# Kernel optimization log

Hardware: AMD Instinct MI355X
Metric: run time of the kernel (lower is better)

Reference implementation:

```python
import jax, jax.numpy as jnp
import numpy as np

TEMPERATURE = 0.07
EPS = 1e-12  # matches torch F.normalize default eps


def setup_inputs() -> dict:
    key = jax.random.key(0)
    k1, k2 = jax.random.split(key)
    features1 = jax.random.normal(k1, (16384, 512), dtype=jnp.float32)
    features2 = jax.random.normal(k2, (16384, 512), dtype=jnp.float32)
    return {"features1": features1, "features2": features2}


def _l2_normalize(x):
    # torch F.normalize: x / max(||x||, eps)
    norm = jnp.sqrt(jnp.sum(x * x, axis=1, keepdims=True))
    return x / jnp.maximum(norm, EPS)


def reference(features1, features2):
    f1 = _l2_normalize(features1)
    f2 = _l2_normalize(features2)
    # [N, N] similarity logits
    logits = jnp.einsum('nd,md->nm', f1, f2) / TEMPERATURE
    n = logits.shape[0]
    # cross-entropy with labels = arange(n): mean over rows of (logsumexp - diag logit)
    log_probs = jax.nn.log_softmax(logits, axis=1)
    diag = jnp.diagonal(log_probs)
    loss = -jnp.mean(diag)
    return loss
```

## Files before the change

### kernel.cpp

```cpp
#include <hip/hip_runtime.h>
#include <stdint.h>

#define NROWS 16384
#define KDIM  512
#define BM 256
#define BN 128
#define CT 4
#define NCHUNK 32
#define NPH 16
#define INV_T 14.285714285714286f
#define LOG2E 1.4426950408889634f
#define LN2   0.6931471805599453f

typedef __bf16 bf16x8 __attribute__((ext_vector_type(8)));
typedef float  f32x16 __attribute__((ext_vector_type(16)));
typedef unsigned short u16x8 __attribute__((ext_vector_type(8)));

__device__ __forceinline__ void gload_lds16(const void* gptr, void* lptr) {
    uint32_t loff = (uint32_t)(uintptr_t)lptr;
    loff = __builtin_amdgcn_readfirstlane(loff);
    __builtin_amdgcn_global_load_lds(
        (const uint32_t __attribute__((address_space(1)))*)(uintptr_t)gptr,
        (uint32_t __attribute__((address_space(3)))*)(uintptr_t)loff,
        16, 0, 0);
}


__global__ void k_norm(const float* __restrict__ X, char* __restrict__ Y, float scale) {
    const int row  = blockIdx.x * 4 + (threadIdx.x >> 6);
    const int lane = threadIdx.x & 63;
    const float* xr = X + (size_t)row * KDIM + lane * 8;
    float4 a = *(const float4*)xr;
    float4 b = *(const float4*)(xr + 4);
    float ss = a.x*a.x + a.y*a.y + a.z*a.z + a.w*a.w
             + b.x*b.x + b.y*b.y + b.z*b.z + b.w*b.w;
    #pragma unroll
    for (int off = 1; off < 64; off <<= 1) ss += __shfl_xor(ss, off);
    const float s = scale / fmaxf(sqrtf(ss), 1e-12f);
    __bf16 o[8];
    o[0] = (__bf16)(a.x * s); o[1] = (__bf16)(a.y * s);
    o[2] = (__bf16)(a.z * s); o[3] = (__bf16)(a.w * s);
    o[4] = (__bf16)(b.x * s); o[5] = (__bf16)(b.y * s);
    o[6] = (__bf16)(b.z * s); o[7] = (__bf16)(b.w * s);
    const int kh = lane >> 2, q = lane & 3;
    const size_t gr = ((size_t)(kh * 512 + (row >> 5)) * 2 + (q >> 1)) * 64
                    + ((q & 1) << 5) + (row & 31);
    *(u16x8*)(Y + gr * 16) = *(const u16x8*)o;
}

__global__ __launch_bounds__(512, 1) void k_gemm(const char* __restrict__ A,
                                                 const char* __restrict__ B,
                                                 float* __restrict__ S_part) {
    __shared__ __align__(16) char L[4 * 24576];
    __shared__ float rowsum[2][BM];
    char* Lc = (char*)L;

    const int tid  = threadIdx.x;
    const int lane = tid & 63;
    const int w    = tid >> 6;
    const int wr   = w >> 1, wc = w & 1;
    const int bid  = blockIdx.x;
    const int xcd  = bid & 7;
    const int idx  = bid >> 3;
    const int st   = idx >> 5;
    const int wsub = idx & 31;
    const int sg   = xcd * 8 + st;
    const int bg   = sg & 7, cg = sg >> 3;
    const int brow  = (bg * 8 + (wsub >> 2)) * BM;
    const int chunk = cg * 4 + (wsub & 3);
    const int rbA0 = brow >> 5;

#define STGA(KH_, S_) do {                                                    \
        const char* g_ = A + ((size_t)((KH_) * 512 + rbA0) * 2048) + tid * 16;\
        char* l_ = Lc + (S_) * 24576 + tid * 16;                              \
        gload_lds16(g_,        l_);                                           \
        gload_lds16(g_ + 8192, l_ + 8192);                                    \
    } while (0)

#define STGB(KH_, S_) do {                                                    \
        const char* g_ = B + ((size_t)((KH_) * 512 + rbB0) * 2048) + tid * 16;\
        char* l_ = Lc + (S_) * 24576 + 16384 + tid * 16;                      \
        gload_lds16(g_, l_);                                                  \
    } while (0)

#define RDS(SET_, HH_) do {                                                   \
        const char* sl_ = Lc + ((HH_) & 3) * 24576;                           \
        _Pragma("unroll") for (int m_ = 0; m_ < 2; ++m_)                      \
        _Pragma("unroll") for (int ks_ = 0; ks_ < 2; ++ks_)                   \
            af[SET_][m_][ks_] = *(const bf16x8*)(sl_ + ((wr * 2 + m_) << 11)  \
                                           + (ks_ << 10) + (lane << 4));      \
        _Pragma("unroll") for (int n_ = 0; n_ < 2; ++n_)                      \
        _Pragma("unroll") for (int ks_ = 0; ks_ < 2; ++ks_)                   \
            bf[SET_][n_][ks_] = *(const bf16x8*)(sl_ + 16384                  \
                  + ((wc * 2 + n_) << 11) + (ks_ << 10) + (lane << 4));       \
    } while (0)

#define MM(SET_) do {                                                         \
        __builtin_amdgcn_s_setprio(1);                                        \
        _Pragma("unroll") for (int m_ = 0; m_ < 2; ++m_)                      \
        _Pragma("unroll") for (int n_ = 0; n_ < 2; ++n_)                      \
        _Pragma("unroll") for (int ks_ = 0; ks_ < 2; ++ks_)                   \
            acc[m_][n_] = __builtin_amdgcn_mfma_f32_32x32x16_bf16(            \
                af[SET_][m_][ks_], bf[SET_][n_][ks_], acc[m_][n_], 0, 0, 0);  \
        __builtin_amdgcn_s_setprio(0);                                        \
    } while (0)

    float rowacc = 0.f;
    #pragma unroll 1
    for (int ct = 0; ct < CT; ++ct) {
        const int rbB0 = (chunk * 16 + ct * 4);
        f32x16 acc[2][2] = {};
        bf16x8 af[2][2][2], bf[2][2][2];

        STGA(0, 0); STGB(0, 0);
        STGA(1, 1); STGB(1, 1);
        STGA(2, 2); STGB(2, 2);
        asm volatile("s_waitcnt vmcnt(3)" ::: "memory");
        __builtin_amdgcn_s_barrier();
        RDS(0, 0);

        #pragma unroll
        for (int h = 0; h < NPH; ++h) {
            if (h < NPH - 1) RDS((h + 1) & 1, h + 1);
            if (h < NPH - 3) { STGA(h + 3, (h + 3) & 3); STGB(h + 3, (h + 3) & 3); }
            MM(h & 1);
            if (h < NPH - 3)       asm volatile("s_waitcnt vmcnt(3)" ::: "memory");
            else if (h == NPH - 3) asm volatile("s_waitcnt vmcnt(0)" ::: "memory");
            __builtin_amdgcn_s_barrier();
        }

        #pragma unroll
        for (int m = 0; m < 2; ++m) {
            float rs[16];
            #pragma unroll
            for (int r = 0; r < 16; ++r)
                rs[r] = __builtin_amdgcn_exp2f(acc[m][0][r])
                      + __builtin_amdgcn_exp2f(acc[m][1][r]);
            #pragma unroll
            for (int off = 16; off >= 1; off >>= 1)
                #pragma unroll
                for (int r = 0; r < 16; ++r)
                    rs[r] += __shfl_xor(rs[r], off);
            if ((lane & 31) == 0) {
                const int rb = wr * 64 + m * 32 + (lane >> 5) * 4;
                #pragma unroll
                for (int r = 0; r < 16; ++r)
                    rowsum[wc][rb + (r & 3) + 8 * (r >> 2)] = rs[r];
            }
        }
        __syncthreads();
        if (tid < BM) rowacc += rowsum[0][tid] + rowsum[1][tid];
        __syncthreads();
    }
#undef STGA
#undef STGB
#undef RDS
#undef MM
    if (tid < BM) S_part[(size_t)chunk * NROWS + brow + tid] = rowacc;
}

__global__ void k_diag(const char* __restrict__ A, const char* __restrict__ B,
                       float* __restrict__ diag) {
    const int row  = blockIdx.x * 4 + (threadIdx.x >> 6);
    const int lane = threadIdx.x & 63;
    const int kh = lane >> 2, q = lane & 3;
    const size_t gr = ((size_t)(kh * 512 + (row >> 5)) * 2 + (q >> 1)) * 64
                    + ((q & 1) << 5) + (row & 31);
    const bf16x8 va = *(const bf16x8*)(A + gr * 16);
    const bf16x8 vb = *(const bf16x8*)(B + gr * 16);
    float d = 0.f;
    #pragma unroll
    for (int i = 0; i < 8; ++i) d += (float)va[i] * (float)vb[i];
    #pragma unroll
    for (int off2 = 1; off2 < 64; off2 <<= 1) d += __shfl_xor(d, off2);
    if (lane == 0) diag[row] = d;
}

__global__ void k_loss(const float* __restrict__ S_part, const float* __restrict__ diag,
                       float* __restrict__ partial) {
    const int g = blockIdx.x * 256 + threadIdx.x;
    float S = 0.f;
    #pragma unroll
    for (int c = 0; c < NCHUNK; ++c) S += S_part[(size_t)c * NROWS + g];
    float v = logf(S) - diag[g] * LN2;
    __shared__ float wsum[4];
    #pragma unroll
    for (int off = 1; off < 64; off <<= 1) v += __shfl_xor(v, off);
    if ((threadIdx.x & 63) == 0) wsum[threadIdx.x >> 6] = v;
    __syncthreads();
    if (threadIdx.x == 0) partial[blockIdx.x] = wsum[0] + wsum[1] + wsum[2] + wsum[3];
}

__global__ void k_final(const float* __restrict__ partial, float* __restrict__ out) {
    float v = partial[threadIdx.x];
    #pragma unroll
    for (int off = 1; off < 64; off <<= 1) v += __shfl_xor(v, off);
    if (threadIdx.x == 0) out[0] = v * (1.0f / (float)NROWS);
}

extern "C" void kernel_launch(void* const* d_in, const int* in_sizes, int n_in,
                              void* d_out, int out_size, void* d_ws, size_t ws_size,
                              hipStream_t stream) {
    const float* f1 = (const float*)d_in[0];
    const float* f2 = (const float*)d_in[1];
    float* out = (float*)d_out;

    char* ws = (char*)d_ws;
    char*  f1p   = ws;
    char*  f2p   = ws + (16u << 20);
    float* S_part = (float*)(ws + (32u << 20));
    float* diag   = (float*)(ws + (34u << 20));
    float* part   = (float*)(ws + (34u << 20) + (1u << 16));

    k_norm<<<dim3(NROWS / 4), dim3(256), 0, stream>>>(f1, f1p, INV_T * LOG2E);
    k_norm<<<dim3(NROWS / 4), dim3(256), 0, stream>>>(f2, f2p, 1.0f);
    k_gemm<<<dim3((NROWS / BM) * NCHUNK), dim3(512), 0, stream>>>(f1p, f2p, S_part);
    k_diag<<<dim3(NROWS / 4), dim3(256), 0, stream>>>(f1p, f2p, diag);
    k_loss<<<dim3(NROWS / 256), dim3(256), 0, stream>>>(S_part, diag, part);
    k_final<<<dim3(1), dim3(64), 0, stream>>>(part, out);
}
```

Before: 358.4 us.

## Reshape GEMM tile to 128x256 with 256-thread blocks, two per CU

```diff
diff --git a/kernel.cpp b/kernel.cpp
--- a/kernel.cpp
+++ b/kernel.cpp
@@ -3,11 +3,12 @@
 
 #define NROWS 16384
 #define KDIM  512
-#define BM 256
-#define BN 128
-#define CT 4
+#define BM 128
+#define BN 256
+#define CT 2
 #define NCHUNK 32
 #define NPH 16
+#define SLOT 24576
 #define INV_T 14.285714285714286f
 #define LOG2E 1.4426950408889634f
 #define LN2   0.6931471805599453f
@@ -48,10 +49,10 @@
     *(u16x8*)(Y + gr * 16) = *(const u16x8*)o;
 }
 
-__global__ __launch_bounds__(512, 1) void k_gemm(const char* __restrict__ A,
+__global__ __launch_bounds__(256, 2) void k_gemm(const char* __restrict__ A,
                                                  const char* __restrict__ B,
                                                  float* __restrict__ S_part) {
-    __shared__ __align__(16) char L[4 * 24576];
+    __shared__ __align__(16) char L[3 * SLOT];
     __shared__ float rowsum[2][BM];
     char* Lc = (char*)L;
 
@@ -64,68 +65,69 @@
     const int idx  = bid >> 3;
     const int st   = idx >> 5;
     const int wsub = idx & 31;
-    const int sg   = xcd * 8 + st;
-    const int bg   = sg & 7, cg = sg >> 3;
+    const int sg   = xcd * 16 + st;
+    const int bg   = sg & 15, cg = sg >> 4;
     const int brow  = (bg * 8 + (wsub >> 2)) * BM;
     const int chunk = cg * 4 + (wsub & 3);
     const int rbA0 = brow >> 5;
 
 #define STGA(KH_, S_) do {                                                    \
         const char* g_ = A + ((size_t)((KH_) * 512 + rbA0) * 2048) + tid * 16;\
-        char* l_ = Lc + (S_) * 24576 + tid * 16;                              \
+        char* l_ = Lc + (S_) * SLOT + tid * 16;                               \
         gload_lds16(g_,        l_);                                           \
-        gload_lds16(g_ + 8192, l_ + 8192);                                    \
+        gload_lds16(g_ + 4096, l_ + 4096);                                    \
     } while (0)
 
 #define STGB(KH_, S_) do {                                                    \
         const char* g_ = B + ((size_t)((KH_) * 512 + rbB0) * 2048) + tid * 16;\
-        char* l_ = Lc + (S_) * 24576 + 16384 + tid * 16;                      \
-        gload_lds16(g_, l_);                                                  \
-    } while (0)
-
-#define RDS(SET_, HH_) do {                                                   \
-        const char* sl_ = Lc + ((HH_) & 3) * 24576;                           \
+        char* l_ = Lc + (S_) * SLOT + 8192 + tid * 16;                        \
+        gload_lds16(g_,         l_);                                          \
+        gload_lds16(g_ +  4096, l_ +  4096);                                  \
+        gload_lds16(g_ +  8192, l_ +  8192);                                  \
+        gload_lds16(g_ + 12288, l_ + 12288);                                  \
+    } while (0)
+
+#define RDS(HH_) do {                                                         \
+        const char* sl_ = Lc + ((HH_) % 3) * SLOT;                            \
         _Pragma("unroll") for (int m_ = 0; m_ < 2; ++m_)                      \
         _Pragma("unroll") for (int ks_ = 0; ks_ < 2; ++ks_)                   \
-            af[SET_][m_][ks_] = *(const bf16x8*)(sl_ + ((wr * 2 + m_) << 11)  \
+            af[m_][ks_] = *(const bf16x8*)(sl_ + ((wr * 2 + m_) << 11)        \
                                            + (ks_ << 10) + (lane << 4));      \
-        _Pragma("unroll") for (int n_ = 0; n_ < 2; ++n_)                      \
+        _Pragma("unroll") for (int n_ = 0; n_ < 4; ++n_)                      \
         _Pragma("unroll") for (int ks_ = 0; ks_ < 2; ++ks_)                   \
-            bf[SET_][n_][ks_] = *(const bf16x8*)(sl_ + 16384                  \
-                  + ((wc * 2 + n_) << 11) + (ks_ << 10) + (lane << 4));       \
-    } while (0)
-
-#define MM(SET_) do {                                                         \
+            bf[n_][ks_] = *(const bf16x8*)(sl_ + 8192                         \
+                  + ((wc * 4 + n_) << 11) + (ks_ << 10) + (lane << 4));       \
+    } while (0)
+
+#define MM() do {                                                             \
         __builtin_amdgcn_s_setprio(1);                                        \
         _Pragma("unroll") for (int m_ = 0; m_ < 2; ++m_)                      \
-        _Pragma("unroll") for (int n_ = 0; n_ < 2; ++n_)                      \
+        _Pragma("unroll") for (int n_ = 0; n_ < 4; ++n_)                      \
         _Pragma("unroll") for (int ks_ = 0; ks_ < 2; ++ks_)                   \
             acc[m_][n_] = __builtin_amdgcn_mfma_f32_32x32x16_bf16(            \
-                af[SET_][m_][ks_], bf[SET_][n_][ks_], acc[m_][n_], 0, 0, 0);  \
+                af[m_][ks_], bf[n_][ks_], acc[m_][n_], 0, 0, 0);              \
         __builtin_amdgcn_s_setprio(0);                                        \
     } while (0)
 
     float rowacc = 0.f;
     #pragma unroll 1
     for (int ct = 0; ct < CT; ++ct) {
-        const int rbB0 = (chunk * 16 + ct * 4);
-        f32x16 acc[2][2] = {};
-        bf16x8 af[2][2][2], bf[2][2][2];
+        const int rbB0 = chunk * 16 + ct * 8;
+        f32x16 acc[2][4] = {};
+        bf16x8 af[2][2], bf[4][2];
 
         STGA(0, 0); STGB(0, 0);
         STGA(1, 1); STGB(1, 1);
-        STGA(2, 2); STGB(2, 2);
-        asm volatile("s_waitcnt vmcnt(3)" ::: "memory");
+        asm volatile("s_waitcnt vmcnt(6)" ::: "memory");
         __builtin_amdgcn_s_barrier();
-        RDS(0, 0);
 
         #pragma unroll
         for (int h = 0; h < NPH; ++h) {
-            if (h < NPH - 1) RDS((h + 1) & 1, h + 1);
-            if (h < NPH - 3) { STGA(h + 3, (h + 3) & 3); STGB(h + 3, (h + 3) & 3); }
-            MM(h & 1);
-            if (h < NPH - 3)       asm volatile("s_waitcnt vmcnt(3)" ::: "memory");
-            else if (h == NPH - 3) asm volatile("s_waitcnt vmcnt(0)" ::: "memory");
+            RDS(h);
+            if (h < NPH - 2) { STGA(h + 2, (h + 2) % 3); STGB(h + 2, (h + 2) % 3); }
+            MM();
+            if (h < NPH - 2)       asm volatile("s_waitcnt vmcnt(6)" ::: "memory");
+            else if (h == NPH - 2) asm volatile("s_waitcnt vmcnt(0)" ::: "memory");
             __builtin_amdgcn_s_barrier();
         }
 
@@ -135,7 +137,9 @@
             #pragma unroll
             for (int r = 0; r < 16; ++r)
                 rs[r] = __builtin_amdgcn_exp2f(acc[m][0][r])
-                      + __builtin_amdgcn_exp2f(acc[m][1][r]);
+                      + __builtin_amdgcn_exp2f(acc[m][1][r])
+                      + __builtin_amdgcn_exp2f(acc[m][2][r])
+                      + __builtin_amdgcn_exp2f(acc[m][3][r]);
             #pragma unroll
             for (int off = 16; off >= 1; off >>= 1)
                 #pragma unroll
@@ -214,7 +218,7 @@
 
     k_norm<<<dim3(NROWS / 4), dim3(256), 0, stream>>>(f1, f1p, INV_T * LOG2E);
     k_norm<<<dim3(NROWS / 4), dim3(256), 0, stream>>>(f2, f2p, 1.0f);
-    k_gemm<<<dim3((NROWS / BM) * NCHUNK), dim3(512), 0, stream>>>(f1p, f2p, S_part);
+    k_gemm<<<dim3((NROWS / BM) * NCHUNK), dim3(256), 0, stream>>>(f1p, f2p, S_part);
     k_diag<<<dim3(NROWS / 4), dim3(256), 0, stream>>>(f1p, f2p, diag);
     k_loss<<<dim3(NROWS / 256), dim3(256), 0, stream>>>(S_part, diag, part);
     k_final<<<dim3(1), dim3(64), 0, stream>>>(part, out);
```

New measurement: 350.2 us. -2.3%, faster.

## Switch similarity GEMM to FP8 MFMA with fp32 diagonal computed from raw inputs

Applied to the files above, without the earlier changes.

```diff
diff --git a/kernel.cpp b/kernel.cpp
--- a/kernel.cpp
+++ b/kernel.cpp
@@ -7,14 +7,14 @@
 #define BN 128
 #define CT 4
 #define NCHUNK 32
-#define NPH 16
+#define NPH 8
+#define SLOT 24576
 #define INV_T 14.285714285714286f
 #define LOG2E 1.4426950408889634f
-#define LN2   0.6931471805599453f
-
-typedef __bf16 bf16x8 __attribute__((ext_vector_type(8)));
-typedef float  f32x16 __attribute__((ext_vector_type(16)));
-typedef unsigned short u16x8 __attribute__((ext_vector_type(8)));
+
+typedef int   i32x4 __attribute__((ext_vector_type(4)));
+typedef int   i32x8 __attribute__((ext_vector_type(8)));
+typedef float f32x16 __attribute__((ext_vector_type(16)));
 
 __device__ __forceinline__ void gload_lds16(const void* gptr, void* lptr) {
     uint32_t loff = (uint32_t)(uintptr_t)lptr;
@@ -23,6 +23,34 @@
         (const uint32_t __attribute__((address_space(1)))*)(uintptr_t)gptr,
         (uint32_t __attribute__((address_space(3)))*)(uintptr_t)loff,
         16, 0, 0);
+}
+
+__device__ __forceinline__ uint32_t f2fp8_manual(float x) {
+    uint32_t b = __float_as_uint(x);
+    uint32_t s = (b >> 31) << 7;
+    uint32_t mag = b & 0x7FFFFFFFu;
+    if (mag >= 0x43E00000u) return s | 0x7Eu;
+    if (mag < 0x3C000000u) {
+        float m = __uint_as_float(mag) * 512.0f;
+        return s | (uint32_t)(m + 0.5f);
+    }
+    uint32_t r = mag + 0x0007FFFFu + ((mag >> 20) & 1u);
+    int e = (int)(r >> 23) - 120;
+    uint32_t m3 = (r >> 20) & 7u;
+    if (e <= 0) { float m = __uint_as_float(mag) * 512.0f; return s | (uint32_t)(m + 0.5f); }
+    if (e > 15 || (e == 15 && m3 == 7)) return s | 0x7Eu;
+    return s | ((uint32_t)e << 3) | m3;
+}
+
+__device__ __forceinline__ uint32_t pack4_fp8(float a, float b, float c, float d) {
+#if __has_builtin(__builtin_amdgcn_cvt_pk_fp8_f32)
+    int w = __builtin_amdgcn_cvt_pk_fp8_f32(a, b, 0, false);
+    w = __builtin_amdgcn_cvt_pk_fp8_f32(c, d, w, true);
+    return (uint32_t)w;
+#else
+    return f2fp8_manual(a) | (f2fp8_manual(b) << 8)
+         | (f2fp8_manual(c) << 16) | (f2fp8_manual(d) << 24);
+#endif
 }
 
 
@@ -37,21 +65,22 @@
     #pragma unroll
     for (int off = 1; off < 64; off <<= 1) ss += __shfl_xor(ss, off);
     const float s = scale / fmaxf(sqrtf(ss), 1e-12f);
-    __bf16 o[8];
-    o[0] = (__bf16)(a.x * s); o[1] = (__bf16)(a.y * s);
-    o[2] = (__bf16)(a.z * s); o[3] = (__bf16)(a.w * s);
-    o[4] = (__bf16)(b.x * s); o[5] = (__bf16)(b.y * s);
-    o[6] = (__bf16)(b.z * s); o[7] = (__bf16)(b.w * s);
-    const int kh = lane >> 2, q = lane & 3;
-    const size_t gr = ((size_t)(kh * 512 + (row >> 5)) * 2 + (q >> 1)) * 64
-                    + ((q & 1) << 5) + (row & 31);
-    *(u16x8*)(Y + gr * 16) = *(const u16x8*)o;
+    uint32_t w0 = pack4_fp8(a.x * s, a.y * s, a.z * s, a.w * s);
+    uint32_t w1 = pack4_fp8(b.x * s, b.y * s, b.z * s, b.w * s);
+    const int kt   = lane >> 3;
+    const int mlan = ((lane >> 2) & 1) * 32 + (row & 31);
+    const int half = (lane >> 1) & 1;
+    const int boff = (lane & 1) * 8;
+    char* dst = Y + ((size_t)(kt * 512 + (row >> 5)) * 2048)
+                  + half * 1024 + mlan * 16 + boff;
+    *(uint32_t*)dst = w0;
+    *(uint32_t*)(dst + 4) = w1;
 }
 
 __global__ __launch_bounds__(512, 1) void k_gemm(const char* __restrict__ A,
                                                  const char* __restrict__ B,
                                                  float* __restrict__ S_part) {
-    __shared__ __align__(16) char L[4 * 24576];
+    __shared__ __align__(16) char L[3 * SLOT];
     __shared__ float rowsum[2][BM];
     char* Lc = (char*)L;
 
@@ -70,62 +99,64 @@
     const int chunk = cg * 4 + (wsub & 3);
     const int rbA0 = brow >> 5;
 
-#define STGA(KH_, S_) do {                                                    \
-        const char* g_ = A + ((size_t)((KH_) * 512 + rbA0) * 2048) + tid * 16;\
-        char* l_ = Lc + (S_) * 24576 + tid * 16;                              \
+#define STGA(KT_, S_) do {                                                    \
+        const char* g_ = A + ((size_t)((KT_) * 512 + rbA0) * 2048) + tid * 16;\
+        char* l_ = Lc + (S_) * SLOT + tid * 16;                               \
         gload_lds16(g_,        l_);                                           \
         gload_lds16(g_ + 8192, l_ + 8192);                                    \
     } while (0)
 
-#define STGB(KH_, S_) do {                                                    \
-        const char* g_ = B + ((size_t)((KH_) * 512 + rbB0) * 2048) + tid * 16;\
-        char* l_ = Lc + (S_) * 24576 + 16384 + tid * 16;                      \
+#define STGB(KT_, S_) do {                                                    \
+        const char* g_ = B + ((size_t)((KT_) * 512 + rbB0) * 2048) + tid * 16;\
+        char* l_ = Lc + (S_) * SLOT + 16384 + tid * 16;                       \
         gload_lds16(g_, l_);                                                  \
     } while (0)
 
-#define RDS(SET_, HH_) do {                                                   \
-        const char* sl_ = Lc + ((HH_) & 3) * 24576;                           \
-        _Pragma("unroll") for (int m_ = 0; m_ < 2; ++m_)                      \
-        _Pragma("unroll") for (int ks_ = 0; ks_ < 2; ++ks_)                   \
-            af[SET_][m_][ks_] = *(const bf16x8*)(sl_ + ((wr * 2 + m_) << 11)  \
-                                           + (ks_ << 10) + (lane << 4));      \
-        _Pragma("unroll") for (int n_ = 0; n_ < 2; ++n_)                      \
-        _Pragma("unroll") for (int ks_ = 0; ks_ < 2; ++ks_)                   \
-            bf[SET_][n_][ks_] = *(const bf16x8*)(sl_ + 16384                  \
-                  + ((wc * 2 + n_) << 11) + (ks_ << 10) + (lane << 4));       \
-    } while (0)
-
-#define MM(SET_) do {                                                         \
+#define RDS(HH_) do {                                                         \
+        const char* sl_ = Lc + ((HH_) % 3) * SLOT;                            \
+        _Pragma("unroll") for (int m_ = 0; m_ < 2; ++m_) {                    \
+            i32x4 lo_ = *(const i32x4*)(sl_ + ((wr * 2 + m_) << 11) + (lane << 4));       \
+            i32x4 hi_ = *(const i32x4*)(sl_ + ((wr * 2 + m_) << 11) + 1024 + (lane << 4));\
+            _Pragma("unroll") for (int j_ = 0; j_ < 4; ++j_) {                \
+                aI[m_][j_] = lo_[j_]; aI[m_][4 + j_] = hi_[j_]; }             \
+        }                                                                     \
+        _Pragma("unroll") for (int n_ = 0; n_ < 2; ++n_) {                    \
+            i32x4 lo_ = *(const i32x4*)(sl_ + 16384 + ((wc * 2 + n_) << 11) + (lane << 4));       \
+            i32x4 hi_ = *(const i32x4*)(sl_ + 16384 + ((wc * 2 + n_) << 11) + 1024 + (lane << 4));\
+            _Pragma("unroll") for (int j_ = 0; j_ < 4; ++j_) {                \
+                bI[n_][j_] = lo_[j_]; bI[n_][4 + j_] = hi_[j_]; }             \
+        }                                                                     \
+    } while (0)
+
+#define MM() do {                                                             \
         __builtin_amdgcn_s_setprio(1);                                        \
         _Pragma("unroll") for (int m_ = 0; m_ < 2; ++m_)                      \
         _Pragma("unroll") for (int n_ = 0; n_ < 2; ++n_)                      \
-        _Pragma("unroll") for (int ks_ = 0; ks_ < 2; ++ks_)                   \
-            acc[m_][n_] = __builtin_amdgcn_mfma_f32_32x32x16_bf16(            \
-                af[SET_][m_][ks_], bf[SET_][n_][ks_], acc[m_][n_], 0, 0, 0);  \
+            acc[m_][n_] = __builtin_amdgcn_mfma_scale_f32_32x32x64_f8f6f4(    \
+                aI[m_], bI[n_], acc[m_][n_], 0, 0,                            \
+                0, 0x7F7F7F7F, 0, 0x7F7F7F7F);                                \
         __builtin_amdgcn_s_setprio(0);                                        \
     } while (0)
 
     float rowacc = 0.f;
     #pragma unroll 1
     for (int ct = 0; ct < CT; ++ct) {
-        const int rbB0 = (chunk * 16 + ct * 4);
+        const int rbB0 = chunk * 16 + ct * 4;
         f32x16 acc[2][2] = {};
-        bf16x8 af[2][2][2], bf[2][2][2];
+        i32x8 aI[2], bI[2];
 
         STGA(0, 0); STGB(0, 0);
         STGA(1, 1); STGB(1, 1);
-        STGA(2, 2); STGB(2, 2);
         asm volatile("s_waitcnt vmcnt(3)" ::: "memory");
         __builtin_amdgcn_s_barrier();
-        RDS(0, 0);
 
         #pragma unroll
         for (int h = 0; h < NPH; ++h) {
-            if (h < NPH - 1) RDS((h + 1) & 1, h + 1);
-            if (h < NPH - 3) { STGA(h + 3, (h + 3) & 3); STGB(h + 3, (h + 3) & 3); }
-            MM(h & 1);
-            if (h < NPH - 3)       asm volatile("s_waitcnt vmcnt(3)" ::: "memory");
-            else if (h == NPH - 3) asm volatile("s_waitcnt vmcnt(0)" ::: "memory");
+            RDS(h);
+            if (h < NPH - 2) { STGA(h + 2, (h + 2) % 3); STGB(h + 2, (h + 2) % 3); }
+            MM();
+            if (h < NPH - 2)       asm volatile("s_waitcnt vmcnt(3)" ::: "memory");
+            else if (h == NPH - 2) asm volatile("s_waitcnt vmcnt(0)" ::: "memory");
             __builtin_amdgcn_s_barrier();
         }
 
@@ -159,21 +190,28 @@
     if (tid < BM) S_part[(size_t)chunk * NROWS + brow + tid] = rowacc;
 }
 
-__global__ void k_diag(const char* __restrict__ A, const char* __restrict__ B,
+__global__ void k_diag(const float* __restrict__ X1, const float* __restrict__ X2,
                        float* __restrict__ diag) {
     const int row  = blockIdx.x * 4 + (threadIdx.x >> 6);
     const int lane = threadIdx.x & 63;
-    const int kh = lane >> 2, q = lane & 3;
-    const size_t gr = ((size_t)(kh * 512 + (row >> 5)) * 2 + (q >> 1)) * 64
-                    + ((q & 1) << 5) + (row & 31);
-    const bf16x8 va = *(const bf16x8*)(A + gr * 16);
-    const bf16x8 vb = *(const bf16x8*)(B + gr * 16);
-    float d = 0.f;
-    #pragma unroll
-    for (int i = 0; i < 8; ++i) d += (float)va[i] * (float)vb[i];
-    #pragma unroll
-    for (int off2 = 1; off2 < 64; off2 <<= 1) d += __shfl_xor(d, off2);
-    if (lane == 0) diag[row] = d;
+    const float* x1 = X1 + (size_t)row * KDIM + lane * 8;
+    const float* x2 = X2 + (size_t)row * KDIM + lane * 8;
+    float4 a0 = *(const float4*)x1, a1 = *(const float4*)(x1 + 4);
+    float4 b0 = *(const float4*)x2, b1 = *(const float4*)(x2 + 4);
+    float s1 = a0.x*a0.x + a0.y*a0.y + a0.z*a0.z + a0.w*a0.w
+             + a1.x*a1.x + a1.y*a1.y + a1.z*a1.z + a1.w*a1.w;
+    float s2 = b0.x*b0.x + b0.y*b0.y + b0.z*b0.z + b0.w*b0.w
+             + b1.x*b1.x + b1.y*b1.y + b1.z*b1.z + b1.w*b1.w;
+    float dd = a0.x*b0.x + a0.y*b0.y + a0.z*b0.z + a0.w*b0.w
+             + a1.x*b1.x + a1.y*b1.y + a1.z*b1.z + a1.w*b1.w;
+    #pragma unroll
+    for (int off = 1; off < 64; off <<= 1) {
+        s1 += __shfl_xor(s1, off);
+        s2 += __shfl_xor(s2, off);
+        dd += __shfl_xor(dd, off);
+    }
+    if (lane == 0)
+        diag[row] = dd / (fmaxf(sqrtf(s1), 1e-12f) * fmaxf(sqrtf(s2), 1e-12f)) * INV_T;
 }
 
 __global__ void k_loss(const float* __restrict__ S_part, const float* __restrict__ diag,
@@ -182,7 +220,7 @@
     float S = 0.f;
     #pragma unroll
     for (int c = 0; c < NCHUNK; ++c) S += S_part[(size_t)c * NROWS + g];
-    float v = logf(S) - diag[g] * LN2;
+    float v = logf(S) - diag[g];
     __shared__ float wsum[4];
     #pragma unroll
     for (int off = 1; off < 64; off <<= 1) v += __shfl_xor(v, off);
@@ -215,7 +253,7 @@
     k_norm<<<dim3(NROWS / 4), dim3(256), 0, stream>>>(f1, f1p, INV_T * LOG2E);
     k_norm<<<dim3(NROWS / 4), dim3(256), 0, stream>>>(f2, f2p, 1.0f);
     k_gemm<<<dim3((NROWS / BM) * NCHUNK), dim3(512), 0, stream>>>(f1p, f2p, S_part);
-    k_diag<<<dim3(NROWS / 4), dim3(256), 0, stream>>>(f1p, f2p, diag);
+    k_diag<<<dim3(NROWS / 4), dim3(256), 0, stream>>>(f1, f2, diag);
     k_loss<<<dim3(NROWS / 256), dim3(256), 0, stream>>>(S_part, diag, part);
     k_final<<<dim3(1), dim3(64), 0, stream>>>(part, out);
 }
```

Result: slower. 522.8 us (+45.9%).
